# Kernel optimization log

Hardware: AMD Instinct MI355X
Metric: run time of the kernel (lower is better)

## Reference

```python
import jax, jax.numpy as jnp
import numpy as np

B, S, D = 8, 4096, 1024
MINR, MAXR = 0.9, 0.999


def setup_inputs() -> dict:
    key = jax.random.key(0)
    ks = jax.random.split(key, 10)

    def dense(k, fin, fout):
        # lecun_normal-style init for flax nn.Dense kernels
        return jax.random.normal(k, (fin, fout), jnp.float32) * (fin ** -0.5)

    x = jax.random.normal(ks[0], (B, S, D), jnp.float32)
    # RNN 'a' param: stable_init -> uniform in [min_rad, max_rad]
    a_fwd = jax.random.uniform(ks[1], (D,), jnp.float32, MINR, MAXR)
    # RGLRU 'a' param: recurrence_init
    u = jax.random.uniform(ks[2], (D,), jnp.float32)
    log_rad = 0.5 * jnp.log(u * (MAXR ** 2 - MINR ** 2) + MINR ** 2)
    a_param = jnp.log(jnp.exp(-log_rad) - 1.0)
    return {
        "x": x,
        "a_fwd": a_fwd,
        "Wf1": dense(ks[3], D, D), "bf1": jnp.zeros((D,), jnp.float32),
        "Wf2": dense(ks[4], D, D), "bf2": jnp.zeros((D,), jnp.float32),
        "Wbx": dense(ks[5], D, D), "bbx": jnp.zeros((D,), jnp.float32),
        "Wgx": dense(ks[6], D, D), "bgx": jnp.zeros((D,), jnp.float32),
        "Wga": dense(ks[7], D, D), "bga": jnp.zeros((D,), jnp.float32),
        "a_param": a_param,
        "Wb2": dense(ks[8], D, D), "bb2": jnp.zeros((D,), jnp.float32),
    }


def reference(x, a_fwd, Wf1, bf1, Wf2, bf2, Wbx, bbx, Wgx, bgx, Wga, bga,
              a_param, Wb2, bb2):
    b = x.shape[0]
    d = Wf1.shape[1]
    identity = x
    xg = jax.nn.gelu(x)  # flax nn.gelu default = tanh approximation

    # ---- forward branch: plain linear RNN  h = a*h + x_t ----
    u = xg @ Wf1 + bf1                       # [B,S,D]
    u_sf = jnp.swapaxes(u, 0, 1)             # [S,B,D]

    def step_f(h, ut):
        h = a_fwd * h + ut
        return h, h

    _, hf = jax.lax.scan(step_f, jnp.zeros((b, d), u.dtype), u_sf)
    out_f = jnp.swapaxes(hf, 0, 1) @ Wf2 + bf2

    # ---- backward branch: RG-LRU, reversed scan ----
    v = xg @ Wbx + bbx                       # [B,S,D]
    gate_x = jax.nn.sigmoid(v @ Wgx + bgx)
    gate_a = jax.nn.sigmoid(v @ Wga + bga)
    log_a = -8.0 * gate_a * jax.nn.softplus(a_param)
    a = jnp.exp(log_a)                       # [B,S,D]
    # h = a*h + sqrt(1 - a^2) * (gate_x * v)
    scaled_in = jnp.sqrt(1.0 - jnp.exp(2.0 * log_a)) * (gate_x * v)

    a_sf = jnp.swapaxes(a, 0, 1)             # [S,B,D]
    in_sf = jnp.swapaxes(scaled_in, 0, 1)    # [S,B,D]

    def step_b(h, inp):
        a_t, g_t = inp
        h = a_t * h + g_t
        return h, h

    _, hb = jax.lax.scan(step_b, jnp.zeros((b, d), v.dtype), (a_sf, in_sf),
                         reverse=True)
    out_b = jnp.swapaxes(hb, 0, 1) @ Wb2 + bb2

    return out_f + out_b + identity
```

## Files before the change

kernel.cpp:

```cpp
#include <hip/hip_runtime.h>

typedef __bf16 bf16;
typedef __bf16 bf16x8 __attribute__((ext_vector_type(8)));
typedef float floatx4 __attribute__((ext_vector_type(4)));

typedef __attribute__((address_space(1))) const void gvoid_t;
typedef __attribute__((address_space(3))) void lvoid_t;

#define B_DIM 8
#define S_DIM 4096
#define M_DIM 32768
#define CHUNK 128
#define NCHUNK 32

__device__ __forceinline__ void gload_lds16(const bf16* g, bf16* l) {
    __builtin_amdgcn_global_load_lds((gvoid_t*)g, (lvoid_t*)l, 16, 0, 0);
}

__device__ __forceinline__ float gelu_tanh(float x) {
    float x3 = x * x * x;
    return 0.5f * x * (1.0f + tanhf(0.7978845608028654f * (x + 0.044715f * x3)));
}

__device__ __forceinline__ float sigmoidf(float z) {
    return 1.0f / (1.0f + expf(-z));
}

__global__ void prep_weights(const float* __restrict__ W0, const float* __restrict__ W1,
                             const float* __restrict__ W2, const float* __restrict__ W3,
                             const float* __restrict__ W4, const float* __restrict__ W5,
                             bf16* __restrict__ T0, bf16* __restrict__ T1,
                             bf16* __restrict__ T2, bf16* __restrict__ T3,
                             bf16* __restrict__ T4, bf16* __restrict__ T5) {
    __shared__ float tile[32][33];
    int mz = blockIdx.z;
    const float* W = mz == 0 ? W0 : mz == 1 ? W1 : mz == 2 ? W2 : mz == 3 ? W3 : mz == 4 ? W4 : W5;
    bf16* T = mz == 0 ? T0 : mz == 1 ? T1 : mz == 2 ? T2 : mz == 3 ? T3 : mz == 4 ? T4 : T5;
    int tn = blockIdx.x * 32;
    int tk = blockIdx.y * 32;
    int tx = threadIdx.x & 31, ty = threadIdx.x >> 5;
#pragma unroll
    for (int i = 0; i < 4; ++i)
        tile[ty + i * 8][tx] = W[(size_t)(tk + ty + i * 8) * 1024 + tn + tx];
    __syncthreads();
#pragma unroll
    for (int i = 0; i < 4; ++i)
        T[(size_t)(tn + ty + i * 8) * 1024 + tk + tx] = (bf16)tile[tx][ty + i * 8];
}

__global__ void sp_kernel(const float* __restrict__ a_param, float* __restrict__ spbuf) {
    int d = blockIdx.x * 256 + threadIdx.x;
    spbuf[d] = log1pf(expf(a_param[d]));
}

__global__ void gelu_kernel(const float* __restrict__ x, bf16* __restrict__ xg) {
    size_t i = (size_t)blockIdx.x * 256 + threadIdx.x;
    float4 v = ((const float4*)x)[i];
    bf16 o0 = (bf16)gelu_tanh(v.x), o1 = (bf16)gelu_tanh(v.y);
    bf16 o2 = (bf16)gelu_tanh(v.z), o3 = (bf16)gelu_tanh(v.w);
    typedef __bf16 bf16x4 __attribute__((ext_vector_type(4)));
    bf16x4 o = {o0, o1, o2, o3};
    ((bf16x4*)xg)[i] = o;
}

template <int MODE>
__launch_bounds__(512, 4)
__global__ void gemm_w(const bf16* __restrict__ A, const bf16* __restrict__ Bt,
                       float* __restrict__ outf, bf16* __restrict__ outh,
                       const float* __restrict__ bias,
                       const float* __restrict__ auxf,
                       const bf16* __restrict__ labuf,
                       const bf16* __restrict__ vbuf) {
    __shared__ __align__(16) bf16 lsA[2][4096];
    __shared__ __align__(16) bf16 lsB[4][4096];
    const int tid = threadIdx.x;
    const int wave = tid >> 6;
    const int lane = tid & 63;
    const int lane15 = lane & 15;
    const int quad = lane >> 4;
    const int wm = wave >> 2;
    const int wn = wave & 3;
    const int blk = blockIdx.x;
    const int xcd = blk & 7;
    const int j = blk >> 3;
    const long m0 = (long)(xcd * 32 + (j >> 2)) * 128;
    const long n0 = (long)(j & 3) * 256;
    const int sr = tid >> 3;
    const int sk8 = (tid & 7) ^ (sr & 7);
    const bf16* gA = A + (size_t)(m0 + sr) * 1024 + sk8 * 8;
    const bf16* gB = Bt + (size_t)(n0 + sr) * 1024 + sk8 * 8;

    floatx4 acc[4][4] = {};

    for (int kt = 0; kt < 16; ++kt) {
        __syncthreads();
        gload_lds16(gA + (size_t)kt * 64, &lsA[0][tid * 8]);
        gload_lds16(gA + (size_t)64 * 1024 + kt * 64, &lsA[1][tid * 8]);
#pragma unroll
        for (int i = 0; i < 4; ++i)
            gload_lds16(gB + (size_t)(i * 64) * 1024 + kt * 64, &lsB[i][tid * 8]);
        __syncthreads();
#pragma unroll
        for (int kk = 0; kk < 2; ++kk) {
            bf16x8 af[4], bfr[4];
#pragma unroll
            for (int mi = 0; mi < 4; ++mi) {
                int rl = mi * 16 + lane15;
                af[mi] = *(const bf16x8*)&lsA[wm][rl * 64 + ((kk * 4 + quad) ^ (rl & 7)) * 8];
            }
#pragma unroll
            for (int ni = 0; ni < 4; ++ni) {
                int rl = ni * 16 + lane15;
                bfr[ni] = *(const bf16x8*)&lsB[wn][rl * 64 + ((kk * 4 + quad) ^ (rl & 7)) * 8];
            }
#pragma unroll
            for (int mi = 0; mi < 4; ++mi)
#pragma unroll
                for (int ni = 0; ni < 4; ++ni)
                    acc[mi][ni] = __builtin_amdgcn_mfma_f32_16x16x32_bf16(af[mi], bfr[ni], acc[mi][ni], 0, 0, 0);
        }
    }

#pragma unroll
    for (int mi = 0; mi < 4; ++mi) {
#pragma unroll
        for (int ni = 0; ni < 4; ++ni) {
            floatx4 v = acc[mi][ni];
            long gn = n0 + wn * 64 + ni * 16 + lane15;
#pragma unroll
            for (int r = 0; r < 4; ++r) {
                long gm = m0 + wm * 64 + mi * 16 + quad * 4 + r;
                size_t o = (size_t)gm * 1024 + gn;
                if (MODE == 0) {
                    outf[o] = v[r] + bias[gn];
                } else if (MODE == 1) {
                    outh[o] = (bf16)(v[r] + bias[gn]);
                } else if (MODE == 2) {
                    float z = v[r] + bias[gn];
                    outh[o] = (bf16)(-8.0f * sigmoidf(z) * auxf[gn]);
                } else {
                    float z = v[r] + bias[gn];
                    float laf = (float)labuf[o];
                    float sc = sqrtf(-expm1f(2.0f * laf)) * sigmoidf(z) * (float)vbuf[o];
                    outh[o] = (bf16)sc;
                }
            }
        }
    }
}

__launch_bounds__(512, 4)
__global__ void gemm_cat(const bf16* __restrict__ A0, const bf16* __restrict__ A1,
                         const bf16* __restrict__ B0t, const bf16* __restrict__ B1t,
                         float* __restrict__ outf,
                         const float* __restrict__ bias0, const float* __restrict__ bias1,
                         const float* __restrict__ xres) {
    __shared__ __align__(16) bf16 lsA[2][4096];
    __shared__ __align__(16) bf16 lsB[4][4096];
    const int tid = threadIdx.x;
    const int wave = tid >> 6;
    const int lane = tid & 63;
    const int lane15 = lane & 15;
    const int quad = lane >> 4;
    const int wm = wave >> 2;
    const int wn = wave & 3;
    const int blk = blockIdx.x;
    const int xcd = blk & 7;
    const int j = blk >> 3;
    const long m0 = (long)(xcd * 32 + (j >> 2)) * 128;
    const long n0 = (long)(j & 3) * 256;
    const int sr = tid >> 3;
    const int sk8 = (tid & 7) ^ (sr & 7);

    floatx4 acc[4][4] = {};

    for (int kt = 0; kt < 32; ++kt) {
        const bf16* Ap = (kt < 16) ? A0 : A1;
        const bf16* Bp = (kt < 16) ? B0t : B1t;
        const int ko = kt & 15;
        const bf16* gA = Ap + (size_t)(m0 + sr) * 1024 + sk8 * 8 + (size_t)ko * 64;
        const bf16* gB = Bp + (size_t)(n0 + sr) * 1024 + sk8 * 8 + (size_t)ko * 64;
        __syncthreads();
        gload_lds16(gA, &lsA[0][tid * 8]);
        gload_lds16(gA + (size_t)64 * 1024, &lsA[1][tid * 8]);
#pragma unroll
        for (int i = 0; i < 4; ++i)
            gload_lds16(gB + (size_t)(i * 64) * 1024, &lsB[i][tid * 8]);
        __syncthreads();
#pragma unroll
        for (int kk = 0; kk < 2; ++kk) {
            bf16x8 af[4], bfr[4];
#pragma unroll
            for (int mi = 0; mi < 4; ++mi) {
                int rl = mi * 16 + lane15;
                af[mi] = *(const bf16x8*)&lsA[wm][rl * 64 + ((kk * 4 + quad) ^ (rl & 7)) * 8];
            }
#pragma unroll
            for (int ni = 0; ni < 4; ++ni) {
                int rl = ni * 16 + lane15;
                bfr[ni] = *(const bf16x8*)&lsB[wn][rl * 64 + ((kk * 4 + quad) ^ (rl & 7)) * 8];
            }
#pragma unroll
            for (int mi = 0; mi < 4; ++mi)
#pragma unroll
                for (int ni = 0; ni < 4; ++ni)
                    acc[mi][ni] = __builtin_amdgcn_mfma_f32_16x16x32_bf16(af[mi], bfr[ni], acc[mi][ni], 0, 0, 0);
        }
    }

#pragma unroll
    for (int mi = 0; mi < 4; ++mi) {
#pragma unroll
        for (int ni = 0; ni < 4; ++ni) {
            floatx4 v = acc[mi][ni];
            long gn = n0 + wn * 64 + ni * 16 + lane15;
#pragma unroll
            for (int r = 0; r < 4; ++r) {
                long gm = m0 + wm * 64 + mi * 16 + quad * 4 + r;
                size_t o = (size_t)gm * 1024 + gn;
                outf[o] = v[r] + bias0[gn] + bias1[gn] + xres[o];
            }
        }
    }
}

__global__ void fscan1(const float* __restrict__ u, const float* __restrict__ a_fwd,
                       float* __restrict__ carry) {
    int d = (blockIdx.x & 3) * 256 + threadIdx.x;
    int c = (blockIdx.x >> 2) & 31;
    int b = blockIdx.x >> 7;
    float a = a_fwd[d];
    const float* up = u + ((size_t)(b * S_DIM + c * CHUNK)) * 1024 + d;
    float h = 0.0f;
#pragma unroll 8
    for (int t = 0; t < CHUNK; ++t) h = fmaf(a, h, up[(size_t)t * 1024]);
    carry[((size_t)c * 8 + b) * 1024 + d] = h;
}
__global__ void fscan2(const float* __restrict__ carry, const float* __restrict__ a_fwd,
                       float* __restrict__ H) {
    int idx = blockIdx.x * 256 + threadIdx.x;
    int d = idx & 1023, b = idx >> 10;
    float a = a_fwd[d];
    float aL = a;
#pragma unroll
    for (int i = 0; i < 7; ++i) aL *= aL;
    float h = 0.0f;
    for (int c = 0; c < NCHUNK; ++c) {
        size_t o = ((size_t)c * 8 + b) * 1024 + d;
        H[o] = h;
        h = fmaf(aL, h, carry[o]);
    }
}
__global__ void fscan3(const float* __restrict__ u, const float* __restrict__ a_fwd,
                       const float* __restrict__ H, bf16* __restrict__ hf) {
    int d = (blockIdx.x & 3) * 256 + threadIdx.x;
    int c = (blockIdx.x >> 2) & 31;
    int b = blockIdx.x >> 7;
    float a = a_fwd[d];
    const float* up = u + ((size_t)(b * S_DIM + c * CHUNK)) * 1024 + d;
    bf16* op = hf + ((size_t)(b * S_DIM + c * CHUNK)) * 1024 + d;
    float h = H[((size_t)c * 8 + b) * 1024 + d];
#pragma unroll 4
    for (int t = 0; t < CHUNK; ++t) {
        h = fmaf(a, h, up[(size_t)t * 1024]);
        op[(size_t)t * 1024] = (bf16)h;
    }
}

__global__ void bscan1(const bf16* __restrict__ la, const bf16* __restrict__ sc,
                       float* __restrict__ BL, float* __restrict__ BP) {
    int d = (blockIdx.x & 3) * 256 + threadIdx.x;
    int c = (blockIdx.x >> 2) & 31;
    int b = blockIdx.x >> 7;
    const bf16* lap = la + ((size_t)(b * S_DIM + c * CHUNK)) * 1024 + d;
    const bf16* gp = sc + ((size_t)(b * S_DIM + c * CHUNK)) * 1024 + d;
    float h = 0.0f, slog = 0.0f;
#pragma unroll 4
    for (int t = CHUNK - 1; t >= 0; --t) {
        float laf = (float)lap[(size_t)t * 1024];
        h = fmaf(expf(laf), h, (float)gp[(size_t)t * 1024]);
        slog += laf;
    }
    size_t o = ((size_t)c * 8 + b) * 1024 + d;
    BL[o] = h;
    BP[o] = expf(slog);
}
__global__ void bscan2(const float* __restrict__ BL, const float* __restrict__ BP,
                       float* __restrict__ R) {
    int idx = blockIdx.x * 256 + threadIdx.x;
    int d = idx & 1023, b = idx >> 10;
    float r = 0.0f;
    for (int c = NCHUNK - 1; c >= 0; --c) {
        size_t o = ((size_t)c * 8 + b) * 1024 + d;
        R[o] = r;
        r = fmaf(BP[o], r, BL[o]);
    }
}
__global__ void bscan3(const bf16* __restrict__ la, const bf16* __restrict__ sc,
                       const float* __restrict__ R, bf16* __restrict__ hb) {
    int d = (blockIdx.x & 3) * 256 + threadIdx.x;
    int c = (blockIdx.x >> 2) & 31;
    int b = blockIdx.x >> 7;
    const bf16* lap = la + ((size_t)(b * S_DIM + c * CHUNK)) * 1024 + d;
    const bf16* gp = sc + ((size_t)(b * S_DIM + c * CHUNK)) * 1024 + d;
    bf16* op = hb + ((size_t)(b * S_DIM + c * CHUNK)) * 1024 + d;
    float h = R[((size_t)c * 8 + b) * 1024 + d];
#pragma unroll 4
    for (int t = CHUNK - 1; t >= 0; --t) {
        h = fmaf(expf((float)lap[(size_t)t * 1024]), h, (float)gp[(size_t)t * 1024]);
        op[(size_t)t * 1024] = (bf16)h;
    }
}

extern "C" void kernel_launch(void* const* d_in, const int* in_sizes, int n_in,
                              void* d_out, int out_size, void* d_ws, size_t ws_size,
                              hipStream_t stream) {
    const float* x       = (const float*)d_in[0];
    const float* a_fwd   = (const float*)d_in[1];
    const float* Wf1     = (const float*)d_in[2];
    const float* bf1     = (const float*)d_in[3];
    const float* Wf2     = (const float*)d_in[4];
    const float* bf2     = (const float*)d_in[5];
    const float* Wbx     = (const float*)d_in[6];
    const float* bbx     = (const float*)d_in[7];
    const float* Wgx     = (const float*)d_in[8];
    const float* bgx     = (const float*)d_in[9];
    const float* Wga     = (const float*)d_in[10];
    const float* bga     = (const float*)d_in[11];
    const float* a_param = (const float*)d_in[12];
    const float* Wb2     = (const float*)d_in[13];
    const float* bb2     = (const float*)d_in[14];
    float* out = (float*)d_out;
    (void)in_sizes; (void)n_in; (void)out_size; (void)ws_size;

    char* ws = (char*)d_ws;
    size_t off = 0;
    const size_t WSZ = (size_t)1024 * 1024 * 2;
    bf16* Wf1t = (bf16*)(ws + off); off += WSZ;
    bf16* Wbxt = (bf16*)(ws + off); off += WSZ;
    bf16* Wgxt = (bf16*)(ws + off); off += WSZ;
    bf16* Wgat = (bf16*)(ws + off); off += WSZ;
    bf16* Wf2t = (bf16*)(ws + off); off += WSZ;
    bf16* Wb2t = (bf16*)(ws + off); off += WSZ;
    float* spbuf = (float*)(ws + off); off += 4096;
    const size_t BSZ = (size_t)M_DIM * 1024 * 2;
    bf16* buf0 = (bf16*)(ws + off); off += BSZ;
    bf16* buf1 = (bf16*)(ws + off); off += BSZ;
    bf16* buf2 = (bf16*)(ws + off); off += BSZ;
    float* Fc = (float*)(ws + off); off += (size_t)NCHUNK * 8 * 1024 * 4;
    float* FH = (float*)(ws + off); off += (size_t)NCHUNK * 8 * 1024 * 4;
    float* BL = (float*)(ws + off); off += (size_t)NCHUNK * 8 * 1024 * 4;
    float* BP = (float*)(ws + off); off += (size_t)NCHUNK * 8 * 1024 * 4;
    float* BR = (float*)(ws + off); off += (size_t)NCHUNK * 8 * 1024 * 4;

    bf16* xg = buf0;
    bf16* hf = buf0;
    bf16* vb = buf1;
    bf16* hb = buf1;
    bf16* la = buf2;
    float* u = (float*)d_out;
    bf16* sc = (bf16*)d_out;

    prep_weights<<<dim3(32, 32, 6), 256, 0, stream>>>(Wf1, Wbx, Wgx, Wga, Wf2, Wb2,
                                                      Wf1t, Wbxt, Wgxt, Wgat, Wf2t, Wb2t);
    sp_kernel<<<4, 256, 0, stream>>>(a_param, spbuf);
    gelu_kernel<<<32768, 256, 0, stream>>>(x, xg);
    gemm_w<0><<<1024, 512, 0, stream>>>(xg, Wf1t, u, nullptr, bf1, nullptr, nullptr, nullptr);
    gemm_w<1><<<1024, 512, 0, stream>>>(xg, Wbxt, nullptr, vb, bbx, nullptr, nullptr, nullptr);
    fscan1<<<1024, 256, 0, stream>>>(u, a_fwd, Fc);
    fscan2<<<32, 256, 0, stream>>>(Fc, a_fwd, FH);
    fscan3<<<1024, 256, 0, stream>>>(u, a_fwd, FH, hf);
    gemm_w<2><<<1024, 512, 0, stream>>>(vb, Wgat, nullptr, la, bga, spbuf, nullptr, nullptr);
    gemm_w<3><<<1024, 512, 0, stream>>>(vb, Wgxt, nullptr, sc, bgx, nullptr, la, vb);
    bscan1<<<1024, 256, 0, stream>>>(la, sc, BL, BP);
    bscan2<<<32, 256, 0, stream>>>(BL, BP, BR);
    bscan3<<<1024, 256, 0, stream>>>(la, sc, BR, hb);
    gemm_cat<<<1024, 512, 0, stream>>>(hf, hb, Wf2t, Wb2t, out, bf2, bb2, x);
}
```

Measured before the change: 906.4 us.

## Fuse Wf1/Wbx GEMMs, store u in bf16, vectorize scans two channels

After: 883.7 us. 1.03x faster.

```diff
diff --git a/kernel.cpp b/kernel.cpp
--- a/kernel.cpp
+++ b/kernel.cpp
@@ -1,6 +1,7 @@
 #include <hip/hip_runtime.h>
 
 typedef __bf16 bf16;
+typedef __bf16 bf16x2 __attribute__((ext_vector_type(2)));
 typedef __bf16 bf16x8 __attribute__((ext_vector_type(8)));
 typedef float floatx4 __attribute__((ext_vector_type(4)));
 
@@ -63,10 +64,83 @@
     ((bf16x4*)xg)[i] = o;
 }
 
+__launch_bounds__(512, 4)
+__global__ void gemm_f01(const bf16* __restrict__ A, const bf16* __restrict__ Bt,
+                         bf16* __restrict__ ubuf, bf16* __restrict__ vbuf,
+                         const float* __restrict__ bias0, const float* __restrict__ bias1) {
+    __shared__ __align__(16) bf16 lsA[2][4096];
+    __shared__ __align__(16) bf16 lsB[4][4096];
+    const int tid = threadIdx.x;
+    const int wave = tid >> 6;
+    const int lane = tid & 63;
+    const int lane15 = lane & 15;
+    const int quad = lane >> 4;
+    const int wm = wave >> 2;
+    const int wn = wave & 3;
+    const int blk = blockIdx.x;
+    const int xcd = blk & 7;
+    const int j = blk >> 3;
+    const long m0 = (long)(xcd * 32 + (j >> 3)) * 128;
+    const long n0 = (long)(j & 7) * 256;
+    const int sr = tid >> 3;
+    const int sk8 = (tid & 7) ^ (sr & 7);
+    const bf16* gA = A + (size_t)(m0 + sr) * 1024 + sk8 * 8;
+    const bf16* gB = Bt + (size_t)(n0 + sr) * 1024 + sk8 * 8;
+
+    floatx4 acc[4][4] = {};
+
+    for (int kt = 0; kt < 16; ++kt) {
+        __syncthreads();
+        gload_lds16(gA + (size_t)kt * 64, &lsA[0][tid * 8]);
+        gload_lds16(gA + (size_t)64 * 1024 + kt * 64, &lsA[1][tid * 8]);
+#pragma unroll
+        for (int i = 0; i < 4; ++i)
+            gload_lds16(gB + (size_t)(i * 64) * 1024 + kt * 64, &lsB[i][tid * 8]);
+        __syncthreads();
+#pragma unroll
+        for (int kk = 0; kk < 2; ++kk) {
+            bf16x8 af[4], bfr[4];
+#pragma unroll
+            for (int mi = 0; mi < 4; ++mi) {
+                int rl = mi * 16 + lane15;
+                af[mi] = *(const bf16x8*)&lsA[wm][rl * 64 + ((kk * 4 + quad) ^ (rl & 7)) * 8];
+            }
+#pragma unroll
+            for (int ni = 0; ni < 4; ++ni) {
+                int rl = ni * 16 + lane15;
+                bfr[ni] = *(const bf16x8*)&lsB[wn][rl * 64 + ((kk * 4 + quad) ^ (rl & 7)) * 8];
+            }
+#pragma unroll
+            for (int mi = 0; mi < 4; ++mi)
+#pragma unroll
+                for (int ni = 0; ni < 4; ++ni)
+                    acc[mi][ni] = __builtin_amdgcn_mfma_f32_16x16x32_bf16(af[mi], bfr[ni], acc[mi][ni], 0, 0, 0);
+        }
+    }
+
+    const bool isU = (n0 < 1024);
+    bf16* outp = isU ? ubuf : vbuf;
+    const float* bp = isU ? bias0 : bias1;
+    const long nb = isU ? n0 : (n0 - 1024);
+#pragma unroll
+    for (int mi = 0; mi < 4; ++mi) {
+#pragma unroll
+        for (int ni = 0; ni < 4; ++ni) {
+            floatx4 v = acc[mi][ni];
+            long gn = nb + wn * 64 + ni * 16 + lane15;
+#pragma unroll
+            for (int r = 0; r < 4; ++r) {
+                long gm = m0 + wm * 64 + mi * 16 + quad * 4 + r;
+                outp[(size_t)gm * 1024 + gn] = (bf16)(v[r] + bp[gn]);
+            }
+        }
+    }
+}
+
 template <int MODE>
 __launch_bounds__(512, 4)
 __global__ void gemm_w(const bf16* __restrict__ A, const bf16* __restrict__ Bt,
-                       float* __restrict__ outf, bf16* __restrict__ outh,
+                       bf16* __restrict__ outh,
                        const float* __restrict__ bias,
                        const float* __restrict__ auxf,
                        const bf16* __restrict__ labuf,
@@ -131,11 +205,7 @@
             for (int r = 0; r < 4; ++r) {
                 long gm = m0 + wm * 64 + mi * 16 + quad * 4 + r;
                 size_t o = (size_t)gm * 1024 + gn;
-                if (MODE == 0) {
-                    outf[o] = v[r] + bias[gn];
-                } else if (MODE == 1) {
-                    outh[o] = (bf16)(v[r] + bias[gn]);
-                } else if (MODE == 2) {
+                if (MODE == 2) {
                     float z = v[r] + bias[gn];
                     outh[o] = (bf16)(-8.0f * sigmoidf(z) * auxf[gn]);
                 } else {
@@ -224,17 +294,24 @@
     }
 }
 
-__global__ void fscan1(const float* __restrict__ u, const float* __restrict__ a_fwd,
+__global__ void fscan1(const bf16* __restrict__ u, const float* __restrict__ a_fwd,
                        float* __restrict__ carry) {
-    int d = (blockIdx.x & 3) * 256 + threadIdx.x;
-    int c = (blockIdx.x >> 2) & 31;
-    int b = blockIdx.x >> 7;
-    float a = a_fwd[d];
-    const float* up = u + ((size_t)(b * S_DIM + c * CHUNK)) * 1024 + d;
-    float h = 0.0f;
+    int dg = blockIdx.x & 1;
+    int c = (blockIdx.x >> 1) & 31;
+    int b = blockIdx.x >> 6;
+    int d = (dg * 256 + threadIdx.x) * 2;
+    float a0 = a_fwd[d], a1 = a_fwd[d + 1];
+    const bf16* up = u + ((size_t)(b * S_DIM + c * CHUNK)) * 1024 + d;
+    float h0 = 0.0f, h1 = 0.0f;
 #pragma unroll 8
-    for (int t = 0; t < CHUNK; ++t) h = fmaf(a, h, up[(size_t)t * 1024]);
-    carry[((size_t)c * 8 + b) * 1024 + d] = h;
+    for (int t = 0; t < CHUNK; ++t) {
+        bf16x2 w = *(const bf16x2*)(up + (size_t)t * 1024);
+        h0 = fmaf(a0, h0, (float)w[0]);
+        h1 = fmaf(a1, h1, (float)w[1]);
+    }
+    size_t o = ((size_t)c * 8 + b) * 1024 + d;
+    carry[o] = h0;
+    carry[o + 1] = h1;
 }
 __global__ void fscan2(const float* __restrict__ carry, const float* __restrict__ a_fwd,
                        float* __restrict__ H) {
@@ -251,39 +328,49 @@
         h = fmaf(aL, h, carry[o]);
     }
 }
-__global__ void fscan3(const float* __restrict__ u, const float* __restrict__ a_fwd,
+__global__ void fscan3(const bf16* __restrict__ u, const float* __restrict__ a_fwd,
                        const float* __restrict__ H, bf16* __restrict__ hf) {
-    int d = (blockIdx.x & 3) * 256 + threadIdx.x;
-    int c = (blockIdx.x >> 2) & 31;
-    int b = blockIdx.x >> 7;
-    float a = a_fwd[d];
-    const float* up = u + ((size_t)(b * S_DIM + c * CHUNK)) * 1024 + d;
+    int dg = blockIdx.x & 1;
+    int c = (blockIdx.x >> 1) & 31;
+    int b = blockIdx.x >> 6;
+    int d = (dg * 256 + threadIdx.x) * 2;
+    float a0 = a_fwd[d], a1 = a_fwd[d + 1];
+    const bf16* up = u + ((size_t)(b * S_DIM + c * CHUNK)) * 1024 + d;
     bf16* op = hf + ((size_t)(b * S_DIM + c * CHUNK)) * 1024 + d;
-    float h = H[((size_t)c * 8 + b) * 1024 + d];
+    size_t ho = ((size_t)c * 8 + b) * 1024 + d;
+    float h0 = H[ho], h1 = H[ho + 1];
 #pragma unroll 4
     for (int t = 0; t < CHUNK; ++t) {
-        h = fmaf(a, h, up[(size_t)t * 1024]);
-        op[(size_t)t * 1024] = (bf16)h;
+        bf16x2 w = *(const bf16x2*)(up + (size_t)t * 1024);
+        h0 = fmaf(a0, h0, (float)w[0]);
+        h1 = fmaf(a1, h1, (float)w[1]);
+        bf16x2 ov; ov[0] = (bf16)h0; ov[1] = (bf16)h1;
+        *(bf16x2*)(op + (size_t)t * 1024) = ov;
     }
 }
 
 __global__ void bscan1(const bf16* __restrict__ la, const bf16* __restrict__ sc,
                        float* __restrict__ BL, float* __restrict__ BP) {
-    int d = (blockIdx.x & 3) * 256 + threadIdx.x;
-    int c = (blockIdx.x >> 2) & 31;
-    int b = blockIdx.x >> 7;
+    int dg = blockIdx.x & 1;
+    int c = (blockIdx.x >> 1) & 31;
+    int b = blockIdx.x >> 6;
+    int d = (dg * 256 + threadIdx.x) * 2;
     const bf16* lap = la + ((size_t)(b * S_DIM + c * CHUNK)) * 1024 + d;
     const bf16* gp = sc + ((size_t)(b * S_DIM + c * CHUNK)) * 1024 + d;
-    float h = 0.0f, slog = 0.0f;
+    float h0 = 0.0f, h1 = 0.0f, s0 = 0.0f, s1 = 0.0f;
 #pragma unroll 4
     for (int t = CHUNK - 1; t >= 0; --t) {
-        float laf = (float)lap[(size_t)t * 1024];
-        h = fmaf(expf(laf), h, (float)gp[(size_t)t * 1024]);
-        slog += laf;
+        bf16x2 lw = *(const bf16x2*)(lap + (size_t)t * 1024);
+        bf16x2 gw = *(const bf16x2*)(gp + (size_t)t * 1024);
+        float l0 = (float)lw[0], l1 = (float)lw[1];
+        h0 = fmaf(expf(l0), h0, (float)gw[0]);
+        h1 = fmaf(expf(l1), h1, (float)gw[1]);
+        s0 += l0;
+        s1 += l1;
     }
     size_t o = ((size_t)c * 8 + b) * 1024 + d;
-    BL[o] = h;
-    BP[o] = expf(slog);
+    BL[o] = h0; BL[o + 1] = h1;
+    BP[o] = expf(s0); BP[o + 1] = expf(s1);
 }
 __global__ void bscan2(const float* __restrict__ BL, const float* __restrict__ BP,
                        float* __restrict__ R) {
@@ -298,17 +385,23 @@
 }
 __global__ void bscan3(const bf16* __restrict__ la, const bf16* __restrict__ sc,
                        const float* __restrict__ R, bf16* __restrict__ hb) {
-    int d = (blockIdx.x & 3) * 256 + threadIdx.x;
-    int c = (blockIdx.x >> 2) & 31;
-    int b = blockIdx.x >> 7;
+    int dg = blockIdx.x & 1;
+    int c = (blockIdx.x >> 1) & 31;
+    int b = blockIdx.x >> 6;
+    int d = (dg * 256 + threadIdx.x) * 2;
     const bf16* lap = la + ((size_t)(b * S_DIM + c * CHUNK)) * 1024 + d;
     const bf16* gp = sc + ((size_t)(b * S_DIM + c * CHUNK)) * 1024 + d;
     bf16* op = hb + ((size_t)(b * S_DIM + c * CHUNK)) * 1024 + d;
-    float h = R[((size_t)c * 8 + b) * 1024 + d];
+    size_t ro = ((size_t)c * 8 + b) * 1024 + d;
+    float h0 = R[ro], h1 = R[ro + 1];
 #pragma unroll 4
     for (int t = CHUNK - 1; t >= 0; --t) {
-        h = fmaf(expf((float)lap[(size_t)t * 1024]), h, (float)gp[(size_t)t * 1024]);
-        op[(size_t)t * 1024] = (bf16)h;
+        bf16x2 lw = *(const bf16x2*)(lap + (size_t)t * 1024);
+        bf16x2 gw = *(const bf16x2*)(gp + (size_t)t * 1024);
+        h0 = fmaf(expf((float)lw[0]), h0, (float)gw[0]);
+        h1 = fmaf(expf((float)lw[1]), h1, (float)gw[1]);
+        bf16x2 ov; ov[0] = (bf16)h0; ov[1] = (bf16)h1;
+        *(bf16x2*)(op + (size_t)t * 1024) = ov;
     }
 }
 
@@ -358,22 +451,21 @@
     bf16* vb = buf1;
     bf16* hb = buf1;
     bf16* la = buf2;
-    float* u = (float*)d_out;
+    bf16* ub = (bf16*)d_out;
     bf16* sc = (bf16*)d_out;
 
     prep_weights<<<dim3(32, 32, 6), 256, 0, stream>>>(Wf1, Wbx, Wgx, Wga, Wf2, Wb2,
                                                       Wf1t, Wbxt, Wgxt, Wgat, Wf2t, Wb2t);
     sp_kernel<<<4, 256, 0, stream>>>(a_param, spbuf);
     gelu_kernel<<<32768, 256, 0, stream>>>(x, xg);
-    gemm_w<0><<<1024, 512, 0, stream>>>(xg, Wf1t, u, nullptr, bf1, nullptr, nullptr, nullptr);
-    gemm_w<1><<<1024, 512, 0, stream>>>(xg, Wbxt, nullptr, vb, bbx, nullptr, nullptr, nullptr);
-    fscan1<<<1024, 256, 0, stream>>>(u, a_fwd, Fc);
+    gemm_f01<<<2048, 512, 0, stream>>>(xg, Wf1t, ub, vb, bf1, bbx);
+    fscan1<<<512, 256, 0, stream>>>(ub, a_fwd, Fc);
     fscan2<<<32, 256, 0, stream>>>(Fc, a_fwd, FH);
-    fscan3<<<1024, 256, 0, stream>>>(u, a_fwd, FH, hf);
-    gemm_w<2><<<1024, 512, 0, stream>>>(vb, Wgat, nullptr, la, bga, spbuf, nullptr, nullptr);
-    gemm_w<3><<<1024, 512, 0, stream>>>(vb, Wgxt, nullptr, sc, bgx, nullptr, la, vb);
-    bscan1<<<1024, 256, 0, stream>>>(la, sc, BL, BP);
+    fscan3<<<512, 256, 0, stream>>>(ub, a_fwd, FH, hf);
+    gemm_w<2><<<1024, 512, 0, stream>>>(vb, Wgat, la, bga, spbuf, nullptr, nullptr);
+    gemm_w<3><<<1024, 512, 0, stream>>>(vb, Wgxt, sc, bgx, nullptr, la, vb);
+    bscan1<<<512, 256, 0, stream>>>(la, sc, BL, BP);
     bscan2<<<32, 256, 0, stream>>>(BL, BP, BR);
-    bscan3<<<1024, 256, 0, stream>>>(la, sc, BR, hb);
+    bscan3<<<512, 256, 0, stream>>>(la, sc, BR, hb);
     gemm_cat<<<1024, 512, 0, stream>>>(hf, hb, Wf2t, Wb2t, out, bf2, bb2, x);
 }
```

## Merge paired GEMMs into N=2048 launches, store u in bf16, vectorize scans

Applied to the files above, without the earlier changes.

New measurement: 1.007 ms. 11.1% more time.

```diff
diff --git a/kernel.cpp b/kernel.cpp
--- a/kernel.cpp
+++ b/kernel.cpp
@@ -1,6 +1,7 @@
 #include <hip/hip_runtime.h>
 
 typedef __bf16 bf16;
+typedef __bf16 bf16x4 __attribute__((ext_vector_type(4)));
 typedef __bf16 bf16x8 __attribute__((ext_vector_type(8)));
 typedef float floatx4 __attribute__((ext_vector_type(4)));
 
@@ -58,19 +59,16 @@
     float4 v = ((const float4*)x)[i];
     bf16 o0 = (bf16)gelu_tanh(v.x), o1 = (bf16)gelu_tanh(v.y);
     bf16 o2 = (bf16)gelu_tanh(v.z), o3 = (bf16)gelu_tanh(v.w);
-    typedef __bf16 bf16x4 __attribute__((ext_vector_type(4)));
     bf16x4 o = {o0, o1, o2, o3};
     ((bf16x4*)xg)[i] = o;
 }
 
-template <int MODE>
+template <int PAIR>
 __launch_bounds__(512, 4)
-__global__ void gemm_w(const bf16* __restrict__ A, const bf16* __restrict__ Bt,
-                       float* __restrict__ outf, bf16* __restrict__ outh,
-                       const float* __restrict__ bias,
-                       const float* __restrict__ auxf,
-                       const bf16* __restrict__ labuf,
-                       const bf16* __restrict__ vbuf) {
+__global__ void gemm_pair(const bf16* __restrict__ A, const bf16* __restrict__ Bt,
+                          bf16* __restrict__ out0, bf16* __restrict__ out1,
+                          const float* __restrict__ bias0, const float* __restrict__ bias1,
+                          const float* __restrict__ sp, const bf16* __restrict__ vbuf) {
     __shared__ __align__(16) bf16 lsA[2][4096];
     __shared__ __align__(16) bf16 lsB[4][4096];
     const int tid = threadIdx.x;
@@ -83,8 +81,8 @@
     const int blk = blockIdx.x;
     const int xcd = blk & 7;
     const int j = blk >> 3;
-    const long m0 = (long)(xcd * 32 + (j >> 2)) * 128;
-    const long n0 = (long)(j & 3) * 256;
+    const long m0 = (long)(xcd * 32 + (j >> 3)) * 128;
+    const long n0 = (long)(j & 7) * 256;
     const int sr = tid >> 3;
     const int sk8 = (tid & 7) ^ (sr & 7);
     const bf16* gA = A + (size_t)(m0 + sr) * 1024 + sk8 * 8;
@@ -121,28 +119,29 @@
         }
     }
 
+    const bool first = (n0 < 1024);
+    bf16* outp = first ? out0 : out1;
+    const float* bp = first ? bias0 : bias1;
+    const long nb = first ? n0 : (n0 - 1024);
 #pragma unroll
     for (int mi = 0; mi < 4; ++mi) {
 #pragma unroll
         for (int ni = 0; ni < 4; ++ni) {
             floatx4 v = acc[mi][ni];
-            long gn = n0 + wn * 64 + ni * 16 + lane15;
+            long gn = nb + wn * 64 + ni * 16 + lane15;
 #pragma unroll
             for (int r = 0; r < 4; ++r) {
                 long gm = m0 + wm * 64 + mi * 16 + quad * 4 + r;
                 size_t o = (size_t)gm * 1024 + gn;
-                if (MODE == 0) {
-                    outf[o] = v[r] + bias[gn];
-                } else if (MODE == 1) {
-                    outh[o] = (bf16)(v[r] + bias[gn]);
-                } else if (MODE == 2) {
-                    float z = v[r] + bias[gn];
-                    outh[o] = (bf16)(-8.0f * sigmoidf(z) * auxf[gn]);
+                float z = v[r] + bp[gn];
+                if (PAIR == 0) {
+                    outp[o] = (bf16)z;
                 } else {
-                    float z = v[r] + bias[gn];
-                    float laf = (float)labuf[o];
-                    float sc = sqrtf(-expm1f(2.0f * laf)) * sigmoidf(z) * (float)vbuf[o];
-                    outh[o] = (bf16)sc;
+                    if (first) {
+                        outp[o] = (bf16)(-8.0f * sigmoidf(z) * sp[gn]);
+                    } else {
+                        outp[o] = (bf16)(sigmoidf(z) * (float)vbuf[o]);
+                    }
                 }
             }
         }
@@ -224,17 +223,24 @@
     }
 }
 
-__global__ void fscan1(const float* __restrict__ u, const float* __restrict__ a_fwd,
+__global__ void fscan1(const bf16* __restrict__ u, const float* __restrict__ a_fwd,
                        float* __restrict__ carry) {
-    int d = (blockIdx.x & 3) * 256 + threadIdx.x;
-    int c = (blockIdx.x >> 2) & 31;
-    int b = blockIdx.x >> 7;
-    float a = a_fwd[d];
-    const float* up = u + ((size_t)(b * S_DIM + c * CHUNK)) * 1024 + d;
-    float h = 0.0f;
-#pragma unroll 8
-    for (int t = 0; t < CHUNK; ++t) h = fmaf(a, h, up[(size_t)t * 1024]);
-    carry[((size_t)c * 8 + b) * 1024 + d] = h;
+    int c = blockIdx.x & 31;
+    int b = blockIdx.x >> 5;
+    int d = threadIdx.x * 4;
+    float4 a = *(const float4*)(a_fwd + d);
+    const bf16* up = u + ((size_t)(b * S_DIM + c * CHUNK)) * 1024 + d;
+    float h0 = 0.0f, h1 = 0.0f, h2 = 0.0f, h3 = 0.0f;
+#pragma unroll 4
+    for (int t = 0; t < CHUNK; ++t) {
+        bf16x4 w = *(const bf16x4*)(up + (size_t)t * 1024);
+        h0 = fmaf(a.x, h0, (float)w[0]);
+        h1 = fmaf(a.y, h1, (float)w[1]);
+        h2 = fmaf(a.z, h2, (float)w[2]);
+        h3 = fmaf(a.w, h3, (float)w[3]);
+    }
+    float4 o = {h0, h1, h2, h3};
+    *(float4*)(carry + ((size_t)c * 8 + b) * 1024 + d) = o;
 }
 __global__ void fscan2(const float* __restrict__ carry, const float* __restrict__ a_fwd,
                        float* __restrict__ H) {
@@ -251,39 +257,52 @@
         h = fmaf(aL, h, carry[o]);
     }
 }
-__global__ void fscan3(const float* __restrict__ u, const float* __restrict__ a_fwd,
+__global__ void fscan3(const bf16* __restrict__ u, const float* __restrict__ a_fwd,
                        const float* __restrict__ H, bf16* __restrict__ hf) {
-    int d = (blockIdx.x & 3) * 256 + threadIdx.x;
-    int c = (blockIdx.x >> 2) & 31;
-    int b = blockIdx.x >> 7;
-    float a = a_fwd[d];
-    const float* up = u + ((size_t)(b * S_DIM + c * CHUNK)) * 1024 + d;
+    int c = blockIdx.x & 31;
+    int b = blockIdx.x >> 5;
+    int d = threadIdx.x * 4;
+    float4 a = *(const float4*)(a_fwd + d);
+    const bf16* up = u + ((size_t)(b * S_DIM + c * CHUNK)) * 1024 + d;
     bf16* op = hf + ((size_t)(b * S_DIM + c * CHUNK)) * 1024 + d;
-    float h = H[((size_t)c * 8 + b) * 1024 + d];
+    float4 h = *(const float4*)(H + ((size_t)c * 8 + b) * 1024 + d);
 #pragma unroll 4
     for (int t = 0; t < CHUNK; ++t) {
-        h = fmaf(a, h, up[(size_t)t * 1024]);
-        op[(size_t)t * 1024] = (bf16)h;
-    }
-}
-
-__global__ void bscan1(const bf16* __restrict__ la, const bf16* __restrict__ sc,
+        bf16x4 w = *(const bf16x4*)(up + (size_t)t * 1024);
+        h.x = fmaf(a.x, h.x, (float)w[0]);
+        h.y = fmaf(a.y, h.y, (float)w[1]);
+        h.z = fmaf(a.z, h.z, (float)w[2]);
+        h.w = fmaf(a.w, h.w, (float)w[3]);
+        bf16x4 ov = {(bf16)h.x, (bf16)h.y, (bf16)h.z, (bf16)h.w};
+        *(bf16x4*)(op + (size_t)t * 1024) = ov;
+    }
+}
+
+__global__ void bscan1(const bf16* __restrict__ la, const bf16* __restrict__ gxv,
                        float* __restrict__ BL, float* __restrict__ BP) {
-    int d = (blockIdx.x & 3) * 256 + threadIdx.x;
-    int c = (blockIdx.x >> 2) & 31;
-    int b = blockIdx.x >> 7;
+    int c = blockIdx.x & 31;
+    int b = blockIdx.x >> 5;
+    int d = threadIdx.x * 4;
     const bf16* lap = la + ((size_t)(b * S_DIM + c * CHUNK)) * 1024 + d;
-    const bf16* gp = sc + ((size_t)(b * S_DIM + c * CHUNK)) * 1024 + d;
-    float h = 0.0f, slog = 0.0f;
+    const bf16* gp = gxv + ((size_t)(b * S_DIM + c * CHUNK)) * 1024 + d;
+    float h0 = 0.0f, h1 = 0.0f, h2 = 0.0f, h3 = 0.0f;
+    float s0 = 0.0f, s1 = 0.0f, s2 = 0.0f, s3 = 0.0f;
 #pragma unroll 4
     for (int t = CHUNK - 1; t >= 0; --t) {
-        float laf = (float)lap[(size_t)t * 1024];
-        h = fmaf(expf(laf), h, (float)gp[(size_t)t * 1024]);
-        slog += laf;
+        bf16x4 lw = *(const bf16x4*)(lap + (size_t)t * 1024);
+        bf16x4 gw = *(const bf16x4*)(gp + (size_t)t * 1024);
+        float l0 = (float)lw[0], l1 = (float)lw[1], l2 = (float)lw[2], l3 = (float)lw[3];
+        h0 = fmaf(expf(l0), h0, sqrtf(-expm1f(2.0f * l0)) * (float)gw[0]);
+        h1 = fmaf(expf(l1), h1, sqrtf(-expm1f(2.0f * l1)) * (float)gw[1]);
+        h2 = fmaf(expf(l2), h2, sqrtf(-expm1f(2.0f * l2)) * (float)gw[2]);
+        h3 = fmaf(expf(l3), h3, sqrtf(-expm1f(2.0f * l3)) * (float)gw[3]);
+        s0 += l0; s1 += l1; s2 += l2; s3 += l3;
     }
     size_t o = ((size_t)c * 8 + b) * 1024 + d;
-    BL[o] = h;
-    BP[o] = expf(slog);
+    float4 hv = {h0, h1, h2, h3};
+    float4 pv = {expf(s0), expf(s1), expf(s2), expf(s3)};
+    *(float4*)(BL + o) = hv;
+    *(float4*)(BP + o) = pv;
 }
 __global__ void bscan2(const float* __restrict__ BL, const float* __restrict__ BP,
                        float* __restrict__ R) {
@@ -296,19 +315,26 @@
         r = fmaf(BP[o], r, BL[o]);
     }
 }
-__global__ void bscan3(const bf16* __restrict__ la, const bf16* __restrict__ sc,
+__global__ void bscan3(const bf16* __restrict__ la, const bf16* __restrict__ gxv,
                        const float* __restrict__ R, bf16* __restrict__ hb) {
-    int d = (blockIdx.x & 3) * 256 + threadIdx.x;
-    int c = (blockIdx.x >> 2) & 31;
-    int b = blockIdx.x >> 7;
+    int c = blockIdx.x & 31;
+    int b = blockIdx.x >> 5;
+    int d = threadIdx.x * 4;
     const bf16* lap = la + ((size_t)(b * S_DIM + c * CHUNK)) * 1024 + d;
-    const bf16* gp = sc + ((size_t)(b * S_DIM + c * CHUNK)) * 1024 + d;
+    const bf16* gp = gxv + ((size_t)(b * S_DIM + c * CHUNK)) * 1024 + d;
     bf16* op = hb + ((size_t)(b * S_DIM + c * CHUNK)) * 1024 + d;
-    float h = R[((size_t)c * 8 + b) * 1024 + d];
+    float4 h = *(const float4*)(R + ((size_t)c * 8 + b) * 1024 + d);
 #pragma unroll 4
     for (int t = CHUNK - 1; t >= 0; --t) {
-        h = fmaf(expf((float)lap[(size_t)t * 1024]), h, (float)gp[(size_t)t * 1024]);
-        op[(size_t)t * 1024] = (bf16)h;
+        bf16x4 lw = *(const bf16x4*)(lap + (size_t)t * 1024);
+        bf16x4 gw = *(const bf16x4*)(gp + (size_t)t * 1024);
+        float l0 = (float)lw[0], l1 = (float)lw[1], l2 = (float)lw[2], l3 = (float)lw[3];
+        h.x = fmaf(expf(l0), h.x, sqrtf(-expm1f(2.0f * l0)) * (float)gw[0]);
+        h.y = fmaf(expf(l1), h.y, sqrtf(-expm1f(2.0f * l1)) * (float)gw[1]);
+        h.z = fmaf(expf(l2), h.z, sqrtf(-expm1f(2.0f * l2)) * (float)gw[2]);
+        h.w = fmaf(expf(l3), h.w, sqrtf(-expm1f(2.0f * l3)) * (float)gw[3]);
+        bf16x4 ov = {(bf16)h.x, (bf16)h.y, (bf16)h.z, (bf16)h.w};
+        *(bf16x4*)(op + (size_t)t * 1024) = ov;
     }
 }
 
@@ -338,8 +364,8 @@
     const size_t WSZ = (size_t)1024 * 1024 * 2;
     bf16* Wf1t = (bf16*)(ws + off); off += WSZ;
     bf16* Wbxt = (bf16*)(ws + off); off += WSZ;
+    bf16* Wgat = (bf16*)(ws + off); off += WSZ;
     bf16* Wgxt = (bf16*)(ws + off); off += WSZ;
-    bf16* Wgat = (bf16*)(ws + off); off += WSZ;
     bf16* Wf2t = (bf16*)(ws + off); off += WSZ;
     bf16* Wb2t = (bf16*)(ws + off); off += WSZ;
     float* spbuf = (float*)(ws + off); off += 4096;
@@ -358,22 +384,20 @@
     bf16* vb = buf1;
     bf16* hb = buf1;
     bf16* la = buf2;
-    float* u = (float*)d_out;
-    bf16* sc = (bf16*)d_out;
-
-    prep_weights<<<dim3(32, 32, 6), 256, 0, stream>>>(Wf1, Wbx, Wgx, Wga, Wf2, Wb2,
-                                                      Wf1t, Wbxt, Wgxt, Wgat, Wf2t, Wb2t);
+    bf16* ub = (bf16*)d_out;
+    bf16* gxv = (bf16*)d_out;
+
+    prep_weights<<<dim3(32, 32, 6), 256, 0, stream>>>(Wf1, Wbx, Wga, Wgx, Wf2, Wb2,
+                                                      Wf1t, Wbxt, Wgat, Wgxt, Wf2t, Wb2t);
     sp_kernel<<<4, 256, 0, stream>>>(a_param, spbuf);
     gelu_kernel<<<32768, 256, 0, stream>>>(x, xg);
-    gemm_w<0><<<1024, 512, 0, stream>>>(xg, Wf1t, u, nullptr, bf1, nullptr, nullptr, nullptr);
-    gemm_w<1><<<1024, 512, 0, stream>>>(xg, Wbxt, nullptr, vb, bbx, nullptr, nullptr, nullptr);
-    fscan1<<<1024, 256, 0, stream>>>(u, a_fwd, Fc);
+    gemm_pair<0><<<2048, 512, 0, stream>>>(xg, Wf1t, ub, vb, bf1, bbx, nullptr, nullptr);
+    fscan1<<<256, 256, 0, stream>>>(ub, a_fwd, Fc);
     fscan2<<<32, 256, 0, stream>>>(Fc, a_fwd, FH);
-    fscan3<<<1024, 256, 0, stream>>>(u, a_fwd, FH, hf);
-    gemm_w<2><<<1024, 512, 0, stream>>>(vb, Wgat, nullptr, la, bga, spbuf, nullptr, nullptr);
-    gemm_w<3><<<1024, 512, 0, stream>>>(vb, Wgxt, nullptr, sc, bgx, nullptr, la, vb);
-    bscan1<<<1024, 256, 0, stream>>>(la, sc, BL, BP);
+    fscan3<<<256, 256, 0, stream>>>(ub, a_fwd, FH, hf);
+    gemm_pair<1><<<2048, 512, 0, stream>>>(vb, Wgat, la, gxv, bga, bgx, spbuf, vb);
+    bscan1<<<256, 256, 0, stream>>>(la, gxv, BL, BP);
     bscan2<<<32, 256, 0, stream>>>(BL, BP, BR);
-    bscan3<<<1024, 256, 0, stream>>>(la, sc, BR, hb);
+    bscan3<<<256, 256, 0, stream>>>(la, gxv, BR, hb);
     gemm_cat<<<1024, 512, 0, stream>>>(hf, hb, Wf2t, Wb2t, out, bf2, bb2, x);
 }
```
